# Kernel tuning notes

Measured on AMD Instinct MI355X. Metric: run time of the kernel, lower is better.

The kernel has to match this reference:

```python
import jax, jax.numpy as jnp
import numpy as np


def setup_inputs() -> dict:
    key = jax.random.key(0)
    k1, k2, k3 = jax.random.split(key, 3)
    B, C, O, NF = 4, 16, 16, 9  # num_flows fixed at 9 (3x3 stencil)
    x = jax.random.normal(k1, (B, C, 450, 480), dtype=jnp.float32)
    combinator = jax.random.normal(k2, (O, C * NF), dtype=jnp.float32) * 0.05
    bias = jax.random.normal(k3, (O,), dtype=jnp.float32) * 0.05
    return {"x": x, "combinator": combinator, "bias": bias}


def reference(x, combinator, bias):
    # Original forward: zero-pad x by 1, gather the 9 shifted copies
    # (dy,dx) in row-major order over {-1,0,1}^2, flatten (flow, channel)
    # flow-major, then matmul with combinator and add bias.
    # out[b,o,h,w] = sum_{i,c} combinator[o, i*C + c] * x[b,c,h+dy_i,w+dx_i]
    # with flow index i = (dy+1)*3 + (dx+1) = ky*3 + kx, this is exactly a
    # 3x3 cross-correlation (padding=1) with weight[o,c,ky,kx] =
    # combinator[o, (ky*3+kx)*C + c].
    O = combinator.shape[0]
    C = x.shape[1]
    w = combinator.reshape(O, 3, 3, C).transpose(0, 3, 1, 2)  # OIHW
    out = jax.lax.conv_general_dilated(
        x, w,
        window_strides=(1, 1),
        padding=((1, 1), (1, 1)),
        dimension_numbers=("NCHW", "OIHW", "NCHW"),
    )
    return out + bias[None, :, None, None]
```

## Files before the change

### kernel.cpp

```cpp
#include <hip/hip_runtime.h>


#define HH 450
#define WW 480
#define BB 4
#define CC 16
#define OO 16
#define WT    96
#define WQN   5
#define WIN   100
#define RSTG  10
#define ROUT  8
#define HG    57
#define NTILE 6
#define ITEMS (2 * RSTG * WIN)
#define HALFI (RSTG * WIN)
#define NBLK  (BB * WQN * HG)

typedef __attribute__((ext_vector_type(8))) short    bf16x8;
typedef __attribute__((ext_vector_type(4))) float    f32x4;
typedef __attribute__((ext_vector_type(4))) unsigned u32x4;

static __device__ __forceinline__ unsigned cvt_pk_bf16(float a, float b) {
    unsigned r;
    asm("v_cvt_pk_bf16_f32 %0, %1, %2" : "=v"(r) : "v"(a), "v"(b));
    return r;
}

__global__ __launch_bounds__(256, 5) void flow_mfma_kernel(
    const float* __restrict__ x, const float* __restrict__ comb,
    const float* __restrict__ bias, float* __restrict__ out)
{
    __shared__ __align__(16) short xs[2][RSTG * WIN][8];

    const int tid  = threadIdx.x;
    const int lane = tid & 63;
    const int wv   = tid >> 6;

    int bid = blockIdx.x;
    int xcd = bid & 7, pos = bid >> 3;
    int L   = (xcd < 4) ? xcd * 143 + pos : 4 * 143 + (xcd - 4) * 142 + pos;
    int hg  = L % HG;
    int t2  = L / HG;
    int wq  = t2 % WQN;
    int b   = t2 / WQN;
    int h0  = hg * ROUT;
    int w0  = wq * WT;

    const int col = lane & 15;
    const int grp = lane >> 4;
    bf16x8 af[5];
    #pragma unroll
    for (int m = 0; m < 5; ++m) {
        int k0 = m * 32 + grp * 8;
        u32x4 p;
        if (k0 < 144) {
            float4 u = *(const float4*)(comb + col * 144 + k0);
            float4 v = *(const float4*)(comb + col * 144 + k0 + 4);
            p[0] = cvt_pk_bf16(u.x, u.y);
            p[1] = cvt_pk_bf16(u.z, u.w);
            p[2] = cvt_pk_bf16(v.x, v.y);
            p[3] = cvt_pk_bf16(v.z, v.w);
        } else {
            p[0] = p[1] = p[2] = p[3] = 0u;
        }
        af[m] = __builtin_bit_cast(bf16x8, p);
    }
    f32x4 bv = *(const f32x4*)(bias + grp * 4);

    auto stage = [&](int s) {
        int ch = (s >= HALFI) ? 1 : 0;
        int r2 = s - ch * HALFI;
        int r  = r2 / WIN;
        int wi = r2 - r * WIN;
        int hy = h0 - 1 + r;
        int w  = w0 + wi - 1;
        u32x4 p;
        if (((unsigned)hy < (unsigned)HH) && ((unsigned)w < (unsigned)WW)) {
            const float* xp = x + (((size_t)(b * CC + ch * 8) * HH + hy) * WW + w);
            float f0 = xp[0];
            float f1 = xp[(size_t)1 * HH * WW];
            float f2 = xp[(size_t)2 * HH * WW];
            float f3 = xp[(size_t)3 * HH * WW];
            float f4 = xp[(size_t)4 * HH * WW];
            float f5 = xp[(size_t)5 * HH * WW];
            float f6 = xp[(size_t)6 * HH * WW];
            float f7 = xp[(size_t)7 * HH * WW];
            p[0] = cvt_pk_bf16(f0, f1);
            p[1] = cvt_pk_bf16(f2, f3);
            p[2] = cvt_pk_bf16(f4, f5);
            p[3] = cvt_pk_bf16(f6, f7);
        } else {
            p[0] = p[1] = p[2] = p[3] = 0u;
        }
        *(u32x4*)(&xs[ch][r2][0]) = p;
    };
    #pragma unroll
    for (int it = 0; it < 7; ++it)
        stage(tid + it * 256);
    if (tid < ITEMS - 7 * 256)
        stage(tid + 7 * 256);
    __syncthreads();

    const int fo = grp >> 1;
    const int ch = grp & 1;
    #pragma unroll
    for (int rr = 0; rr < 2; ++rr) {
        int r = 2 * wv + rr;
        int h = h0 + r;
        if (h >= HH) continue;

        int boff[5];
        #pragma unroll
        for (int m = 0; m < 4; ++m) {
            int i  = 2 * m + fo;
            int ky = i / 3;
            int kx = i % 3;
            boff[m] = (r + ky) * WIN + col + kx;
        }
        boff[4] = (r + 2) * WIN + col + 2;

        #pragma unroll
        for (int t = 0; t < NTILE; ++t) {
            int n0 = t * 16;
            f32x4 acc = bv;
            #pragma unroll
            for (int m = 0; m < 4; ++m) {
                bf16x8 bf = *(const bf16x8*)(&xs[ch][boff[m] + n0][0]);
                acc = __builtin_amdgcn_mfma_f32_16x16x32_bf16(af[m], bf, acc, 0, 0, 0);
            }
            bf16x8 b4;
            if (grp < 2) {
                b4 = *(const bf16x8*)(&xs[ch][boff[4] + n0][0]);
            } else {
                #pragma unroll
                for (int j = 0; j < 8; ++j) b4[j] = 0;
            }
            acc = __builtin_amdgcn_mfma_f32_16x16x32_bf16(af[4], b4, acc, 0, 0, 0);

            float* op = out + (((size_t)(b * OO + grp * 4) * HH + h) * WW + w0 + n0 + col);
            #pragma unroll
            for (int j = 0; j < 4; ++j)
                op[(size_t)j * HH * WW] = acc[j];
        }
    }
}

extern "C" void kernel_launch(void* const* d_in, const int* in_sizes, int n_in,
                              void* d_out, int out_size, void* d_ws, size_t ws_size,
                              hipStream_t stream) {
    const float* x    = (const float*)d_in[0];
    const float* comb = (const float*)d_in[1];
    const float* bias = (const float*)d_in[2];
    float* out        = (float*)d_out;

    flow_mfma_kernel<<<NBLK, 256, 0, stream>>>(x, comb, bias, out);
}
```

Measured before the change: 26.38 us.

## Software-pipeline row groups with double-buffered LDS staging per block

Each block now processes four 4-row output groups instead of one 8-row group. The next group's input is loaded into registers while MFMA compute runs on the current LDS buffer, then converted to bf16 and written to the alternate buffer. This is meant to hide global-load latency behind compute and to amortise weight setup over more work. In exchange it uses more registers and LDS, lowers occupancy (launch bounds 5 to 4), launches fewer blocks, and restages halo rows for each small group.

```diff
diff --git a/kernel.cpp b/kernel.cpp
--- a/kernel.cpp
+++ b/kernel.cpp
@@ -9,13 +9,14 @@
 #define WT    96
 #define WQN   5
 #define WIN   100
-#define RSTG  10
-#define ROUT  8
-#define HG    57
+#define RSTG  6
+#define ROUT  4
+#define GPB   4
+#define RBN   29
 #define NTILE 6
 #define ITEMS (2 * RSTG * WIN)
 #define HALFI (RSTG * WIN)
-#define NBLK  (BB * WQN * HG)
+#define NBLK  (BB * WQN * RBN)
 
 typedef __attribute__((ext_vector_type(8))) short    bf16x8;
 typedef __attribute__((ext_vector_type(4))) float    f32x4;
@@ -27,11 +28,11 @@
     return r;
 }
 
-__global__ __launch_bounds__(256, 5) void flow_mfma_kernel(
+__global__ __launch_bounds__(256, 4) void flow_mfma_kernel(
     const float* __restrict__ x, const float* __restrict__ comb,
     const float* __restrict__ bias, float* __restrict__ out)
 {
-    __shared__ __align__(16) short xs[2][RSTG * WIN][8];
+    __shared__ __align__(16) short xs[2][2][RSTG * WIN][8];
 
     const int tid  = threadIdx.x;
     const int lane = tid & 63;
@@ -39,12 +40,11 @@
 
     int bid = blockIdx.x;
     int xcd = bid & 7, pos = bid >> 3;
-    int L   = (xcd < 4) ? xcd * 143 + pos : 4 * 143 + (xcd - 4) * 142 + pos;
-    int hg  = L % HG;
-    int t2  = L / HG;
+    int L   = (xcd < 4) ? xcd * 73 + pos : 4 * 73 + (xcd - 4) * 72 + pos;
+    int rb  = L % RBN;
+    int t2  = L / RBN;
     int wq  = t2 % WQN;
     int b   = t2 / WQN;
-    int h0  = hg * ROUT;
     int w0  = wq * WT;
 
     const int col = lane & 15;
@@ -68,70 +68,76 @@
     }
     f32x4 bv = *(const f32x4*)(bias + grp * 4);
 
-    auto stage = [&](int s) {
-        int ch = (s >= HALFI) ? 1 : 0;
-        int r2 = s - ch * HALFI;
-        int r  = r2 / WIN;
-        int wi = r2 - r * WIN;
-        int hy = h0 - 1 + r;
-        int w  = w0 + wi - 1;
-        u32x4 p;
-        if (((unsigned)hy < (unsigned)HH) && ((unsigned)w < (unsigned)WW)) {
-            const float* xp = x + (((size_t)(b * CC + ch * 8) * HH + hy) * WW + w);
-            float f0 = xp[0];
-            float f1 = xp[(size_t)1 * HH * WW];
-            float f2 = xp[(size_t)2 * HH * WW];
-            float f3 = xp[(size_t)3 * HH * WW];
-            float f4 = xp[(size_t)4 * HH * WW];
-            float f5 = xp[(size_t)5 * HH * WW];
-            float f6 = xp[(size_t)6 * HH * WW];
-            float f7 = xp[(size_t)7 * HH * WW];
-            p[0] = cvt_pk_bf16(f0, f1);
-            p[1] = cvt_pk_bf16(f2, f3);
-            p[2] = cvt_pk_bf16(f4, f5);
-            p[3] = cvt_pk_bf16(f6, f7);
-        } else {
-            p[0] = p[1] = p[2] = p[3] = 0u;
-        }
-        *(u32x4*)(&xs[ch][r2][0]) = p;
-    };
-    #pragma unroll
-    for (int it = 0; it < 7; ++it)
-        stage(tid + it * 256);
-    if (tid < ITEMS - 7 * 256)
-        stage(tid + 7 * 256);
-    __syncthreads();
-
     const int fo = grp >> 1;
     const int ch = grp & 1;
+    int boff[5];
     #pragma unroll
-    for (int rr = 0; rr < 2; ++rr) {
-        int r = 2 * wv + rr;
-        int h = h0 + r;
-        if (h >= HH) continue;
+    for (int m = 0; m < 4; ++m) {
+        int i  = 2 * m + fo;
+        int ky = i / 3;
+        int kx = i % 3;
+        boff[m] = (wv + ky) * WIN + col + kx;
+    }
+    boff[4] = (wv + 2) * WIN + col + 2;
 
-        int boff[5];
+    float fv[5][8];
+
+    auto stage_load = [&](int g) {
+        int h0 = (rb * GPB + g) * ROUT;
         #pragma unroll
-        for (int m = 0; m < 4; ++m) {
-            int i  = 2 * m + fo;
-            int ky = i / 3;
-            int kx = i % 3;
-            boff[m] = (r + ky) * WIN + col + kx;
+        for (int it = 0; it < 5; ++it) {
+            int s = tid + it * 256;
+            bool okit = (s < ITEMS);
+            int chs = (s >= HALFI) ? 1 : 0;
+            int r2  = s - chs * HALFI;
+            int r   = r2 / WIN;
+            int wi  = r2 - r * WIN;
+            int hy  = h0 - 1 + r;
+            int w   = w0 + wi - 1;
+            if (okit && ((unsigned)hy < (unsigned)HH) && ((unsigned)w < (unsigned)WW)) {
+                const float* xp = x + (((size_t)(b * CC + chs * 8) * HH + hy) * WW + w);
+                #pragma unroll
+                for (int j = 0; j < 8; ++j)
+                    fv[it][j] = xp[(size_t)j * HH * WW];
+            } else {
+                #pragma unroll
+                for (int j = 0; j < 8; ++j) fv[it][j] = 0.0f;
+            }
         }
-        boff[4] = (r + 2) * WIN + col + 2;
+    };
 
+    auto stage_write = [&](int buf) {
+        #pragma unroll
+        for (int it = 0; it < 5; ++it) {
+            int s = tid + it * 256;
+            if (s < ITEMS) {
+                int chs = (s >= HALFI) ? 1 : 0;
+                int r2  = s - chs * HALFI;
+                u32x4 p;
+                p[0] = cvt_pk_bf16(fv[it][0], fv[it][1]);
+                p[1] = cvt_pk_bf16(fv[it][2], fv[it][3]);
+                p[2] = cvt_pk_bf16(fv[it][4], fv[it][5]);
+                p[3] = cvt_pk_bf16(fv[it][6], fv[it][7]);
+                *(u32x4*)(&xs[buf][chs][r2][0]) = p;
+            }
+        }
+    };
+
+    auto compute = [&](int g, int buf) {
+        int h = (rb * GPB + g) * ROUT + wv;
+        if (h >= HH) return;
         #pragma unroll
         for (int t = 0; t < NTILE; ++t) {
             int n0 = t * 16;
             f32x4 acc = bv;
             #pragma unroll
             for (int m = 0; m < 4; ++m) {
-                bf16x8 bf = *(const bf16x8*)(&xs[ch][boff[m] + n0][0]);
+                bf16x8 bf = *(const bf16x8*)(&xs[buf][ch][boff[m] + n0][0]);
                 acc = __builtin_amdgcn_mfma_f32_16x16x32_bf16(af[m], bf, acc, 0, 0, 0);
             }
             bf16x8 b4;
             if (grp < 2) {
-                b4 = *(const bf16x8*)(&xs[ch][boff[4] + n0][0]);
+                b4 = *(const bf16x8*)(&xs[buf][ch][boff[4] + n0][0]);
             } else {
                 #pragma unroll
                 for (int j = 0; j < 8; ++j) b4[j] = 0;
@@ -143,6 +149,17 @@
             for (int j = 0; j < 4; ++j)
                 op[(size_t)j * HH * WW] = acc[j];
         }
+    };
+
+    stage_load(0);
+    stage_write(0);
+    __syncthreads();
+    #pragma unroll
+    for (int g = 0; g < GPB; ++g) {
+        if (g + 1 < GPB) stage_load(g + 1);
+        compute(g, g & 1);
+        if (g + 1 < GPB) stage_write((g + 1) & 1);
+        __syncthreads();
     }
 }
 
```

After: 30.04 us. +13.9%, slower.

## Use taller row tiles and paired float2 global loads for staging

Applied to the files above, without the earlier changes.

Each block now computes 12 output rows instead of 8, staging 14 halo rows rather than 10, which cuts the fraction of redundant halo rows loaded. The staging window is widened to 104 columns and starts 4 columns earlier so each thread reads aligned float2 pairs per channel and writes two LDS entries, halving the number of load instructions. Compute offsets gain +3 to match the shifted window. Occupancy drops from 5 to 3 blocks per SIMD bound because of the larger LDS tile, and the XCD block remapping is simplified for the new 760-block grid.

```diff
diff --git a/kernel.cpp b/kernel.cpp
--- a/kernel.cpp
+++ b/kernel.cpp
@@ -8,13 +8,14 @@
 #define OO 16
 #define WT    96
 #define WQN   5
-#define WIN   100
-#define RSTG  10
-#define ROUT  8
-#define HG    57
+#define WIN   104
+#define RSTG  14
+#define ROUT  12
+#define HG    38
 #define NTILE 6
-#define ITEMS (2 * RSTG * WIN)
-#define HALFI (RSTG * WIN)
+#define W2N   (WIN / 2)
+#define HALFI (RSTG * W2N)
+#define ITEMS (2 * HALFI)
 #define NBLK  (BB * WQN * HG)
 
 typedef __attribute__((ext_vector_type(8))) short    bf16x8;
@@ -27,7 +28,7 @@
     return r;
 }
 
-__global__ __launch_bounds__(256, 5) void flow_mfma_kernel(
+__global__ __launch_bounds__(256, 3) void flow_mfma_kernel(
     const float* __restrict__ x, const float* __restrict__ comb,
     const float* __restrict__ bias, float* __restrict__ out)
 {
@@ -38,8 +39,7 @@
     const int wv   = tid >> 6;
 
     int bid = blockIdx.x;
-    int xcd = bid & 7, pos = bid >> 3;
-    int L   = (xcd < 4) ? xcd * 143 + pos : 4 * 143 + (xcd - 4) * 142 + pos;
+    int L   = (bid & 7) * 95 + (bid >> 3);
     int hg  = L % HG;
     int t2  = L / HG;
     int wq  = t2 % WQN;
@@ -69,44 +69,49 @@
     f32x4 bv = *(const f32x4*)(bias + grp * 4);
 
     auto stage = [&](int s) {
-        int ch = (s >= HALFI) ? 1 : 0;
-        int r2 = s - ch * HALFI;
-        int r  = r2 / WIN;
-        int wi = r2 - r * WIN;
-        int hy = h0 - 1 + r;
-        int w  = w0 + wi - 1;
-        u32x4 p;
+        int ch  = (s >= HALFI) ? 1 : 0;
+        int rem = s - ch * HALFI;
+        int r   = rem / W2N;
+        int wi2 = rem - r * W2N;
+        int hy  = h0 - 1 + r;
+        int w   = w0 - 4 + wi2 * 2;
+        u32x4 p0, p1;
         if (((unsigned)hy < (unsigned)HH) && ((unsigned)w < (unsigned)WW)) {
             const float* xp = x + (((size_t)(b * CC + ch * 8) * HH + hy) * WW + w);
-            float f0 = xp[0];
-            float f1 = xp[(size_t)1 * HH * WW];
-            float f2 = xp[(size_t)2 * HH * WW];
-            float f3 = xp[(size_t)3 * HH * WW];
-            float f4 = xp[(size_t)4 * HH * WW];
-            float f5 = xp[(size_t)5 * HH * WW];
-            float f6 = xp[(size_t)6 * HH * WW];
-            float f7 = xp[(size_t)7 * HH * WW];
-            p[0] = cvt_pk_bf16(f0, f1);
-            p[1] = cvt_pk_bf16(f2, f3);
-            p[2] = cvt_pk_bf16(f4, f5);
-            p[3] = cvt_pk_bf16(f6, f7);
+            float fx[8], fy[8];
+            #pragma unroll
+            for (int j = 0; j < 8; ++j) {
+                float2 v = *(const float2*)(xp + (size_t)j * HH * WW);
+                fx[j] = v.x; fy[j] = v.y;
+            }
+            p0[0] = cvt_pk_bf16(fx[0], fx[1]);
+            p0[1] = cvt_pk_bf16(fx[2], fx[3]);
+            p0[2] = cvt_pk_bf16(fx[4], fx[5]);
+            p0[3] = cvt_pk_bf16(fx[6], fx[7]);
+            p1[0] = cvt_pk_bf16(fy[0], fy[1]);
+            p1[1] = cvt_pk_bf16(fy[2], fy[3]);
+            p1[2] = cvt_pk_bf16(fy[4], fy[5]);
+            p1[3] = cvt_pk_bf16(fy[6], fy[7]);
         } else {
-            p[0] = p[1] = p[2] = p[3] = 0u;
+            p0[0] = p0[1] = p0[2] = p0[3] = 0u;
+            p1[0] = p1[1] = p1[2] = p1[3] = 0u;
         }
-        *(u32x4*)(&xs[ch][r2][0]) = p;
+        int r2 = r * WIN + wi2 * 2;
+        *(u32x4*)(&xs[ch][r2][0])     = p0;
+        *(u32x4*)(&xs[ch][r2 + 1][0]) = p1;
     };
     #pragma unroll
-    for (int it = 0; it < 7; ++it)
+    for (int it = 0; it < 5; ++it)
         stage(tid + it * 256);
-    if (tid < ITEMS - 7 * 256)
-        stage(tid + 7 * 256);
+    if (tid < ITEMS - 5 * 256)
+        stage(tid + 5 * 256);
     __syncthreads();
 
     const int fo = grp >> 1;
     const int ch = grp & 1;
     #pragma unroll
-    for (int rr = 0; rr < 2; ++rr) {
-        int r = 2 * wv + rr;
+    for (int rr = 0; rr < 3; ++rr) {
+        int r = 3 * wv + rr;
         int h = h0 + r;
         if (h >= HH) continue;
 
@@ -116,9 +121,9 @@
             int i  = 2 * m + fo;
             int ky = i / 3;
             int kx = i % 3;
-            boff[m] = (r + ky) * WIN + col + kx;
+            boff[m] = (r + ky) * WIN + col + kx + 3;
         }
-        boff[4] = (r + 2) * WIN + col + 2;
+        boff[4] = (r + 2) * WIN + col + 2 + 3;
 
         #pragma unroll
         for (int t = 0; t < NTILE; ++t) {
```

New measurement: 25.04 us, median of 2. 5.1% less time.

## Stage input with float4 loads and retile to 6-row blocks

Applied to the files above, without the earlier changes.

Staging now reads four consecutive pixels per channel with float4 loads and writes four bf16x8 LDS entries per thread, instead of one scalar load per channel per pixel. The halo window widens to 104 columns so each row is loaded in aligned groups of four. Output tiles shrink to 6 rows, giving 75 row groups, and the 36 row-by-tile items are spread evenly over 4 waves. Occupancy is raised to 6 blocks. The intent is fewer global load instructions and better load balance, at the cost of more blocks, more halo overhead and higher register pressure from eight float4 loads per thread.

```diff
diff --git a/kernel.cpp b/kernel.cpp
--- a/kernel.cpp
+++ b/kernel.cpp
@@ -8,13 +8,15 @@
 #define OO 16
 #define WT    96
 #define WQN   5
-#define WIN   100
-#define RSTG  10
-#define ROUT  8
-#define HG    57
+#define WIN   104
+#define RSTG  8
+#define ROUT  6
+#define HG    75
 #define NTILE 6
-#define ITEMS (2 * RSTG * WIN)
-#define HALFI (RSTG * WIN)
+#define W4N   26
+#define HALF  (RSTG * W4N)
+#define ITEMS (2 * HALF)
+#define PLANE (RSTG * WIN)
 #define NBLK  (BB * WQN * HG)
 
 typedef __attribute__((ext_vector_type(8))) short    bf16x8;
@@ -27,11 +29,11 @@
     return r;
 }
 
-__global__ __launch_bounds__(256, 5) void flow_mfma_kernel(
+__global__ __launch_bounds__(256, 6) void flow_mfma_kernel(
     const float* __restrict__ x, const float* __restrict__ comb,
     const float* __restrict__ bias, float* __restrict__ out)
 {
-    __shared__ __align__(16) short xs[2][RSTG * WIN][8];
+    __shared__ __align__(16) short xs[2 * PLANE][8];
 
     const int tid  = threadIdx.x;
     const int lane = tid & 63;
@@ -39,7 +41,7 @@
 
     int bid = blockIdx.x;
     int xcd = bid & 7, pos = bid >> 3;
-    int L   = (xcd < 4) ? xcd * 143 + pos : 4 * 143 + (xcd - 4) * 142 + pos;
+    int L   = (xcd < 4) ? xcd * 188 + pos : 4 * 188 + (xcd - 4) * 187 + pos;
     int hg  = L % HG;
     int t2  = L / HG;
     int wq  = t2 % WQN;
@@ -69,80 +71,80 @@
     f32x4 bv = *(const f32x4*)(bias + grp * 4);
 
     auto stage = [&](int s) {
-        int ch = (s >= HALFI) ? 1 : 0;
-        int r2 = s - ch * HALFI;
-        int r  = r2 / WIN;
-        int wi = r2 - r * WIN;
-        int hy = h0 - 1 + r;
-        int w  = w0 + wi - 1;
-        u32x4 p;
+        int cs  = (s >= HALF) ? 1 : 0;
+        int rem = s - cs * HALF;
+        int r   = rem / W4N;
+        int wi4 = rem - r * W4N;
+        int hy  = h0 - 1 + r;
+        int w   = w0 - 4 + wi4 * 4;
+        u32x4 p[4];
         if (((unsigned)hy < (unsigned)HH) && ((unsigned)w < (unsigned)WW)) {
-            const float* xp = x + (((size_t)(b * CC + ch * 8) * HH + hy) * WW + w);
-            float f0 = xp[0];
-            float f1 = xp[(size_t)1 * HH * WW];
-            float f2 = xp[(size_t)2 * HH * WW];
-            float f3 = xp[(size_t)3 * HH * WW];
-            float f4 = xp[(size_t)4 * HH * WW];
-            float f5 = xp[(size_t)5 * HH * WW];
-            float f6 = xp[(size_t)6 * HH * WW];
-            float f7 = xp[(size_t)7 * HH * WW];
-            p[0] = cvt_pk_bf16(f0, f1);
-            p[1] = cvt_pk_bf16(f2, f3);
-            p[2] = cvt_pk_bf16(f4, f5);
-            p[3] = cvt_pk_bf16(f6, f7);
+            const float* xp = x + (((size_t)(b * CC + cs * 8) * HH + hy) * WW + w);
+            float4 v[8];
+            #pragma unroll
+            for (int j = 0; j < 8; ++j)
+                v[j] = *(const float4*)(xp + (size_t)j * HH * WW);
+            #pragma unroll
+            for (int q = 0; q < 4; ++q) {
+                p[0][q] = cvt_pk_bf16(v[2*q].x, v[2*q+1].x);
+                p[1][q] = cvt_pk_bf16(v[2*q].y, v[2*q+1].y);
+                p[2][q] = cvt_pk_bf16(v[2*q].z, v[2*q+1].z);
+                p[3][q] = cvt_pk_bf16(v[2*q].w, v[2*q+1].w);
+            }
         } else {
-            p[0] = p[1] = p[2] = p[3] = 0u;
+            #pragma unroll
+            for (int k = 0; k < 4; ++k)
+                p[k][0] = p[k][1] = p[k][2] = p[k][3] = 0u;
         }
-        *(u32x4*)(&xs[ch][r2][0]) = p;
+        int r2 = cs * PLANE + r * WIN + wi4 * 4;
+        #pragma unroll
+        for (int k = 0; k < 4; ++k)
+            *(u32x4*)(&xs[r2 + k][0]) = p[k];
     };
-    #pragma unroll
-    for (int it = 0; it < 7; ++it)
-        stage(tid + it * 256);
-    if (tid < ITEMS - 7 * 256)
-        stage(tid + 7 * 256);
+    stage(tid);
+    if (tid < ITEMS - 256)
+        stage(tid + 256);
     __syncthreads();
 
     const int fo = grp >> 1;
     const int ch = grp & 1;
+    int cof[5];
     #pragma unroll
-    for (int rr = 0; rr < 2; ++rr) {
-        int r = 2 * wv + rr;
-        int h = h0 + r;
-        if (h >= HH) continue;
+    for (int m = 0; m < 4; ++m) {
+        int i  = 2 * m + fo;
+        int ky = i / 3;
+        int kx = i - ky * 3;
+        cof[m] = ch * PLANE + ky * WIN + col + kx + 3;
+    }
+    cof[4] = ch * PLANE + 2 * WIN + col + 5;
 
-        int boff[5];
+    #pragma unroll
+    for (int k = 0; k < 9; ++k) {
+        int idx = wv + 4 * k;
+        int row = idx / 6;
+        int t   = idx - row * 6;
+        int h   = h0 + row;
+        int n0  = t * 16;
+        int rbase = row * WIN + n0;
+        f32x4 acc = bv;
         #pragma unroll
         for (int m = 0; m < 4; ++m) {
-            int i  = 2 * m + fo;
-            int ky = i / 3;
-            int kx = i % 3;
-            boff[m] = (r + ky) * WIN + col + kx;
+            bf16x8 bf = *(const bf16x8*)(&xs[rbase + cof[m]][0]);
+            acc = __builtin_amdgcn_mfma_f32_16x16x32_bf16(af[m], bf, acc, 0, 0, 0);
         }
-        boff[4] = (r + 2) * WIN + col + 2;
+        bf16x8 b4;
+        if (grp < 2) {
+            b4 = *(const bf16x8*)(&xs[rbase + cof[4]][0]);
+        } else {
+            #pragma unroll
+            for (int j = 0; j < 8; ++j) b4[j] = 0;
+        }
+        acc = __builtin_amdgcn_mfma_f32_16x16x32_bf16(af[4], b4, acc, 0, 0, 0);
 
+        float* op = out + (((size_t)(b * OO + grp * 4) * HH + h) * WW + w0 + n0 + col);
         #pragma unroll
-        for (int t = 0; t < NTILE; ++t) {
-            int n0 = t * 16;
-            f32x4 acc = bv;
-            #pragma unroll
-            for (int m = 0; m < 4; ++m) {
-                bf16x8 bf = *(const bf16x8*)(&xs[ch][boff[m] + n0][0]);
-                acc = __builtin_amdgcn_mfma_f32_16x16x32_bf16(af[m], bf, acc, 0, 0, 0);
-            }
-            bf16x8 b4;
-            if (grp < 2) {
-                b4 = *(const bf16x8*)(&xs[ch][boff[4] + n0][0]);
-            } else {
-                #pragma unroll
-                for (int j = 0; j < 8; ++j) b4[j] = 0;
-            }
-            acc = __builtin_amdgcn_mfma_f32_16x16x32_bf16(af[4], b4, acc, 0, 0, 0);
-
-            float* op = out + (((size_t)(b * OO + grp * 4) * HH + h) * WW + w0 + n0 + col);
-            #pragma unroll
-            for (int j = 0; j < 4; ++j)
-                op[(size_t)j * HH * WW] = acc[j];
-        }
+        for (int j = 0; j < 4; ++j)
+            op[(size_t)j * HH * WW] = acc[j];
     }
 }
 
```

After: 26.47 us. About the same (+0.4%).
